# Performance work log

Hardware: AMD Instinct MI355X
Metric: run time of the kernel (lower is better)

The kernel has to match this reference:

```python
import jax, jax.numpy as jnp
import numpy as np

C = 32
KSHAPE = (C, C, 3, 3)  # (C_out, C_in, kH, kW)
BN_EPS = 1e-5


def _binary_act(x):
    # forward: sign(x); backward: identity clipped to |x|<1 (STE)
    xc = jnp.clip(x, -1.0, 1.0)
    return jax.lax.stop_gradient(jnp.sign(x) - xc) + xc


def _binarize_weight(w_flat, shape):
    w = w_flat.reshape(shape)
    scale = jax.lax.stop_gradient(jnp.mean(jnp.abs(w)))  # global scalar scale, detached
    wc = jnp.clip(w, -1.0, 1.0)
    # forward: scale*sign(w); backward flows through clamp(w,-1,1)
    return jax.lax.stop_gradient(scale * jnp.sign(w) - wc) + wc


def _bi_conv_bn(x, w_flat, gamma, beta, stride):
    xb = _binary_act(x)
    w = _binarize_weight(w_flat, KSHAPE)
    y = jax.lax.conv_general_dilated(
        xb, w, window_strides=(stride, stride), padding=[(1, 1), (1, 1)],
        dimension_numbers=('NCHW', 'OIHW', 'NCHW'))
    # BatchNorm2d in training mode (batch stats, biased variance)
    m = jnp.mean(y, axis=(0, 2, 3), keepdims=True)
    v = jnp.mean((y - m) ** 2, axis=(0, 2, 3), keepdims=True)
    yhat = (y - m) * jax.lax.rsqrt(v + BN_EPS)
    return gamma.reshape(1, -1, 1, 1) * yhat + beta.reshape(1, -1, 1, 1)


def setup_inputs() -> dict:
    key = jax.random.key(0)
    k1, k2, k3 = jax.random.split(key, 3)
    return {
        'x': jax.random.normal(k1, (32, C, 160, 160), dtype=jnp.float32),
        'w1': jax.random.normal(k2, (C * C * 9, 1), dtype=jnp.float32) * 0.05,
        'gamma1': jnp.ones((C,), dtype=jnp.float32),
        'beta1': jnp.zeros((C,), dtype=jnp.float32),
        'w2': jax.random.normal(k3, (C * C * 9, 1), dtype=jnp.float32) * 0.05,
        'gamma2': jnp.ones((C,), dtype=jnp.float32),
        'beta2': jnp.zeros((C,), dtype=jnp.float32),
    }


def reference(x, w1, gamma1, beta1, w2, gamma2, beta2):
    # bireal residual block, stride=1 => skip_op is Identity
    inner = _bi_conv_bn(x, w1, gamma1, beta1, 1) + x
    out = _bi_conv_bn(inner, w2, gamma2, beta2, 1) + inner
    return out
```

## Files before the change

kernel.cpp:

```cpp
#include <hip/hip_runtime.h>
#include <stdint.h>

#define NIMG 32
#define CH 32
#define HH 160
#define WW 160
#define HWL (HH*WW)
#define PRS 164
#define PHH 162
#define PIMG (PHH*PRS)
#define NPIX (NIMG*HWL)
#define HALO_WORDS 968

#define OFF_P     0
#define OFF_P2    3400704
#define OFF_INNER (OFF_P2 + 3400704)
#define OFF_WP    (OFF_INNER + 52428800)
#define OFF_CORR  (OFF_WP + 2304)
#define OFF_SC    (OFF_CORR + 2304)
#define OFF_SB    (OFF_SC + 128)

struct StatLine {
  int s1; int pad0; unsigned long long s2; char pad[112];
};

#define AS1 __attribute__((address_space(1)))
#define AS3 __attribute__((address_space(3)))
__device__ __forceinline__ void dma16(const void* g, void* l) {
  __builtin_amdgcn_global_load_lds((const AS1 void*)g, (AS3 void*)l, 16, 0, 0);
}

__device__ __forceinline__ unsigned short f2bf(float f) {
  unsigned u = __float_as_uint(f);
  u += 0x7fffu + ((u >> 16) & 1u);
  return (unsigned short)(u >> 16);
}
__device__ __forceinline__ float bf2f(unsigned short u) {
  return __uint_as_float((uint32_t)u << 16);
}

__device__ __forceinline__ void conv4(const uint32_t r[3][6], const uint32_t* wsh,
                                      int co, int& a0, int& a1, int& a2, int& a3)
{
  a0 = a1 = a2 = a3 = 0;
  #pragma unroll
  for (int dy = 0; dy < 3; ++dy) {
    #pragma unroll
    for (int dx = 0; dx < 3; ++dx) {
      uint32_t wvv = wsh[co * 9 + dy * 3 + dx];
      a0 += __popc(r[dy][0 + dx] ^ wvv);
      a1 += __popc(r[dy][1 + dx] ^ wvv);
      a2 += __popc(r[dy][2 + dx] ^ wvv);
      a3 += __popc(r[dy][3 + dx] ^ wvv);
    }
  }
}

__global__ __launch_bounds__(256) void pack_prep(const float* __restrict__ x,
    const float* __restrict__ w1, const float* __restrict__ w2,
    uint32_t* __restrict__ P, uint32_t* __restrict__ P2, uint32_t* __restrict__ WP,
    int* __restrict__ CORR, float* __restrict__ SC, StatLine* __restrict__ SB)
{
  __shared__ float lds[8192];
  const int tid = threadIdx.x;
  const int b = blockIdx.x;

  if (b >= 3200) {
    if (b == 3442) {
      int* z = (int*)SB;
      for (int i = tid; i < 2048; i += 256) z[i] = 0;
      float* red = lds;
      uint32_t* wpl = (uint32_t*)(lds + 256);
      for (int cv = 0; cv < 2; ++cv) {
        const float* w = cv ? w2 : w1;
        float s = 0.f;
        #pragma unroll
        for (int j = 0; j < 9; ++j) {
          float4 v = *reinterpret_cast<const float4*>(w + (j * 256 + tid) * 4);
          s += fabsf(v.x) + fabsf(v.y) + fabsf(v.z) + fabsf(v.w);
        }
        red[tid] = s;
        __syncthreads();
        for (int st = 128; st > 0; st >>= 1) {
          if (tid < st) red[tid] += red[tid + st];
          __syncthreads();
        }
        if (tid == 0) SC[cv] = red[0] / 9216.0f;
        for (int i = tid; i < 288; i += 256) {
          int co = i / 9, t = i - co * 9;
          uint32_t bw = 0;
          for (int ci = 0; ci < 32; ++ci)
            bw |= (w[(co * 32 + ci) * 9 + t] > 0.0f) ? (1u << ci) : 0u;
          WP[cv * 288 + i] = bw;
          wpl[i] = bw;
        }
        __syncthreads();
        for (int i = tid; i < 288; i += 256) {
          int cls = i / 32, co = i - cls * 32;
          int hc = cls / 3, wc = cls - hc * 3;
          int corr = 0;
          for (int t = 0; t < 9; ++t) {
            int dy = t / 3 - 1, dx = t % 3 - 1;
            bool inval = (hc == 0 && dy == -1) || (hc == 2 && dy == 1) ||
                         (wc == 0 && dx == -1) || (wc == 2 && dx == 1);
            if (inval) corr += 32 - 2 * __popc(wpl[co * 9 + t]);
          }
          CORR[cv * 288 + cls * 32 + co] = corr;
        }
        __syncthreads();
      }
    } else {
      int k = (b - 3200) * 256 + tid;
      uint32_t* buf = (k < 32 * HALO_WORDS) ? P : P2;
      int j = k % (32 * HALO_WORDS);
      int img = j / HALO_WORDS;
      int r = j - img * HALO_WORDS;
      int pr, pc;
      if (r < 164)      { pr = 0;   pc = r; }
      else if (r < 328) { pr = 161; pc = r - 164; }
      else {
        int k2 = r - 328;
        pr = 1 + (k2 >> 2);
        int q = k2 & 3;
        pc = (q == 0) ? 0 : (160 + q);
      }
      buf[img * PIMG + pr * PRS + pc] = 0;
    }
    return;
  }

  int n = b / 100;
  int p0 = (b - n * 100) * 256;
  const float* xb = x + (size_t)n * CH * HWL + p0;
  #pragma unroll
  for (int it = 0; it < 8; ++it) {
    int c = it * 4 + (tid >> 6);
    const float* g = xb + (size_t)c * HWL + (tid & 63) * 4;
    dma16(g, lds + c * 256);
  }
  __syncthreads();

  uint32_t bits = 0;
  #pragma unroll
  for (int c = 0; c < 32; ++c) {
    if (lds[c * 256 + tid] > 0.f) bits |= 1u << c;
  }
  int px = p0 + tid;
  int h = px / WW, w = px - h * WW;
  P[n * PIMG + (h + 1) * PRS + (w + 1)] = bits;
}

__global__ __launch_bounds__(256) void conv_stats(const uint32_t* __restrict__ P,
    const uint32_t* __restrict__ WP, const int* __restrict__ CORR,
    StatLine* __restrict__ sb)
{
  __shared__ uint32_t wsh[288];
  __shared__ int csh[288];
  __shared__ int ls1[32], ls2[32];
  const int tid = threadIdx.x;
  for (int i = tid; i < 288; i += 256) { wsh[i] = WP[i]; csh[i] = CORR[i]; }
  if (tid < 32) { ls1[tid] = 0; ls2[tid] = 0; }
  __syncthreads();

  int g = blockIdx.x * 256 + tid;
  int w4 = g % 40;
  int t1 = g / 40;
  int h = t1 % 160;
  int n = t1 / 160;

  const uint32_t* base = P + n * PIMG + h * PRS + w4 * 4;
  uint32_t r[3][6];
  #pragma unroll
  for (int dy = 0; dy < 3; ++dy) {
    uint4 a = *reinterpret_cast<const uint4*>(base + dy * PRS);
    uint2 bw = *reinterpret_cast<const uint2*>(base + dy * PRS + 4);
    r[dy][0] = a.x; r[dy][1] = a.y; r[dy][2] = a.z; r[dy][3] = a.w;
    r[dy][4] = bw.x; r[dy][5] = bw.y;
  }

  int rowc = (h == 0) ? 0 : ((h == 159) ? 6 : 3);
  int cls0  = rowc + ((w4 == 0) ? 0 : 1);
  int cls12 = rowc + 1;
  int cls3  = rowc + ((w4 == 39) ? 2 : 1);
  int lane = tid & 63;

  #pragma unroll
  for (int co = 0; co < 32; ++co) {
    int a0, a1, a2, a3;
    conv4(r, wsh, co, a0, a1, a2, a3);
    int d0 = 288 - 2 * a0 - csh[cls0 * 32 + co];
    int d1 = 288 - 2 * a1 - csh[cls12 * 32 + co];
    int d2 = 288 - 2 * a2 - csh[cls12 * 32 + co];
    int d3 = 288 - 2 * a3 - csh[cls3 * 32 + co];
    int ds = d0 + d1 + d2 + d3;
    int sq = d0 * d0 + d1 * d1 + d2 * d2 + d3 * d3;
    #pragma unroll
    for (int off = 32; off > 0; off >>= 1) {
      ds += __shfl_down(ds, off);
      sq += __shfl_down(sq, off);
    }
    if (lane == 0) { atomicAdd(&ls1[co], ds); atomicAdd(&ls2[co], sq); }
  }
  __syncthreads();
  if (tid < 32) {
    atomicAdd(&sb[tid].s1, ls1[tid]);
    atomicAdd(&sb[tid].s2, (unsigned long long)(long long)ls2[tid]);
  }
}

__global__ __launch_bounds__(256, 2) void conv_bn1(const uint32_t* __restrict__ P,
    const uint32_t* __restrict__ WP, const int* __restrict__ CORR,
    const float* __restrict__ x, const float* __restrict__ SCp,
    const StatLine* __restrict__ sb, const float* __restrict__ gamma,
    const float* __restrict__ beta, unsigned short* __restrict__ INNER,
    uint32_t* __restrict__ P2)
{
  __shared__ uint32_t wsh[288];
  __shared__ int csh[288];
  __shared__ float Ash[32], Bsh[32];
  const int tid = threadIdx.x;
  for (int i = tid; i < 288; i += 256) { wsh[i] = WP[i]; csh[i] = CORR[i]; }
  if (tid < 32) {
    double sc = (double)SCp[0];
    double m  = sc * (double)sb[tid].s1 / (double)NPIX;
    double ms = sc * sc * (double)(long long)sb[tid].s2 / (double)NPIX;
    float inv = (float)(1.0 / sqrt(ms - m * m + 1e-5));
    float gm = gamma[tid];
    Ash[tid] = gm * inv * (float)sc;
    Bsh[tid] = beta[tid] - gm * inv * (float)m;
  }
  __syncthreads();

  int g = blockIdx.x * 256 + tid;
  int w4 = g % 40;
  int t1 = g / 40;
  int h = t1 % 160;
  int n = t1 / 160;

  const uint32_t* base = P + n * PIMG + h * PRS + w4 * 4;
  uint32_t r[3][6];
  #pragma unroll
  for (int dy = 0; dy < 3; ++dy) {
    uint4 a = *reinterpret_cast<const uint4*>(base + dy * PRS);
    uint2 bw = *reinterpret_cast<const uint2*>(base + dy * PRS + 4);
    r[dy][0] = a.x; r[dy][1] = a.y; r[dy][2] = a.z; r[dy][3] = a.w;
    r[dy][4] = bw.x; r[dy][5] = bw.y;
  }
  int rowc = (h == 0) ? 0 : ((h == 159) ? 6 : 3);
  int cls0  = rowc + ((w4 == 0) ? 0 : 1);
  int cls12 = rowc + 1;
  int cls3  = rowc + ((w4 == 39) ? 2 : 1);

  int i = h * WW + w4 * 4;
  size_t pbase = (size_t)n * CH * HWL + i;

  float4 xv[32];
  #pragma unroll
  for (int j = 0; j < 32; ++j)
    xv[j] = *reinterpret_cast<const float4*>(x + pbase + (size_t)j * HWL);

  uint32_t bb0 = 0, bb1 = 0, bb2 = 0, bb3 = 0;
  #pragma unroll
  for (int co = 0; co < 32; ++co) {
    int a0, a1, a2, a3;
    conv4(r, wsh, co, a0, a1, a2, a3);
    int d0 = 288 - 2 * a0 - csh[cls0 * 32 + co];
    int d1 = 288 - 2 * a1 - csh[cls12 * 32 + co];
    int d2 = 288 - 2 * a2 - csh[cls12 * 32 + co];
    int d3 = 288 - 2 * a3 - csh[cls3 * 32 + co];
    float A = Ash[co], Bv = Bsh[co];
    float v0 = fmaf(A, (float)d0, Bv) + xv[co].x;
    float v1 = fmaf(A, (float)d1, Bv) + xv[co].y;
    float v2 = fmaf(A, (float)d2, Bv) + xv[co].z;
    float v3 = fmaf(A, (float)d3, Bv) + xv[co].w;
    ushort4 o; o.x = f2bf(v0); o.y = f2bf(v1); o.z = f2bf(v2); o.w = f2bf(v3);
    *reinterpret_cast<ushort4*>(INNER + pbase + (size_t)co * HWL) = o;
    uint32_t m = 1u << co;
    if (v0 > 0.f) bb0 |= m;
    if (v1 > 0.f) bb1 |= m;
    if (v2 > 0.f) bb2 |= m;
    if (v3 > 0.f) bb3 |= m;
  }
  uint32_t* pw = P2 + n * PIMG + (h + 1) * PRS + (w4 * 4 + 1);
  pw[0] = bb0; pw[1] = bb1; pw[2] = bb2; pw[3] = bb3;
}

__global__ __launch_bounds__(256, 2) void conv_bn2(const uint32_t* __restrict__ P2,
    const uint32_t* __restrict__ WP, const int* __restrict__ CORR,
    const unsigned short* __restrict__ INNER, const float* __restrict__ SCp,
    const StatLine* __restrict__ sb, const float* __restrict__ gamma,
    const float* __restrict__ beta, float* __restrict__ out)
{
  __shared__ uint32_t wsh[288];
  __shared__ int csh[288];
  __shared__ float Ash[32], Bsh[32];
  const int tid = threadIdx.x;
  for (int i = tid; i < 288; i += 256) { wsh[i] = WP[i]; csh[i] = CORR[i]; }
  if (tid < 32) {
    double sc = (double)SCp[0];
    double m  = sc * (double)sb[tid].s1 / (double)NPIX;
    double ms = sc * sc * (double)(long long)sb[tid].s2 / (double)NPIX;
    float inv = (float)(1.0 / sqrt(ms - m * m + 1e-5));
    float gm = gamma[tid];
    Ash[tid] = gm * inv * (float)sc;
    Bsh[tid] = beta[tid] - gm * inv * (float)m;
  }
  __syncthreads();

  int g = blockIdx.x * 256 + tid;
  int w4 = g % 40;
  int t1 = g / 40;
  int h = t1 % 160;
  int n = t1 / 160;

  const uint32_t* base = P2 + n * PIMG + h * PRS + w4 * 4;
  uint32_t r[3][6];
  #pragma unroll
  for (int dy = 0; dy < 3; ++dy) {
    uint4 a = *reinterpret_cast<const uint4*>(base + dy * PRS);
    uint2 bw = *reinterpret_cast<const uint2*>(base + dy * PRS + 4);
    r[dy][0] = a.x; r[dy][1] = a.y; r[dy][2] = a.z; r[dy][3] = a.w;
    r[dy][4] = bw.x; r[dy][5] = bw.y;
  }
  int rowc = (h == 0) ? 0 : ((h == 159) ? 6 : 3);
  int cls0  = rowc + ((w4 == 0) ? 0 : 1);
  int cls12 = rowc + 1;
  int cls3  = rowc + ((w4 == 39) ? 2 : 1);

  int i = h * WW + w4 * 4;
  size_t pbase = (size_t)n * CH * HWL + i;

  ushort4 iv[32];
  #pragma unroll
  for (int j = 0; j < 32; ++j)
    iv[j] = *reinterpret_cast<const ushort4*>(INNER + pbase + (size_t)j * HWL);

  #pragma unroll
  for (int co = 0; co < 32; ++co) {
    int a0, a1, a2, a3;
    conv4(r, wsh, co, a0, a1, a2, a3);
    int d0 = 288 - 2 * a0 - csh[cls0 * 32 + co];
    int d1 = 288 - 2 * a1 - csh[cls12 * 32 + co];
    int d2 = 288 - 2 * a2 - csh[cls12 * 32 + co];
    int d3 = 288 - 2 * a3 - csh[cls3 * 32 + co];
    float A = Ash[co], Bv = Bsh[co];
    float4 o;
    o.x = fmaf(A, (float)d0, Bv) + bf2f(iv[co].x);
    o.y = fmaf(A, (float)d1, Bv) + bf2f(iv[co].y);
    o.z = fmaf(A, (float)d2, Bv) + bf2f(iv[co].z);
    o.w = fmaf(A, (float)d3, Bv) + bf2f(iv[co].w);
    *reinterpret_cast<float4*>(out + pbase + (size_t)co * HWL) = o;
  }
}

extern "C" void kernel_launch(void* const* d_in, const int* in_sizes, int n_in,
                              void* d_out, int out_size, void* d_ws, size_t ws_size,
                              hipStream_t stream)
{
  (void)in_sizes; (void)n_in; (void)out_size; (void)ws_size;
  const float* x  = (const float*)d_in[0];
  const float* w1 = (const float*)d_in[1];
  const float* g1 = (const float*)d_in[2];
  const float* b1 = (const float*)d_in[3];
  const float* w2 = (const float*)d_in[4];
  const float* g2 = (const float*)d_in[5];
  const float* b2 = (const float*)d_in[6];
  float* out = (float*)d_out;
  char* ws = (char*)d_ws;

  uint32_t*       P     = (uint32_t*)(ws + OFF_P);
  uint32_t*       P2    = (uint32_t*)(ws + OFF_P2);
  unsigned short* INNER = (unsigned short*)(ws + OFF_INNER);
  uint32_t*       WP    = (uint32_t*)(ws + OFF_WP);
  int*            CORR  = (int*)(ws + OFF_CORR);
  float*          SC    = (float*)(ws + OFF_SC);
  StatLine*       SB    = (StatLine*)(ws + OFF_SB);

  pack_prep<<<3443, 256, 0, stream>>>(x, w1, w2, P, P2, WP, CORR, SC, SB);
  conv_stats<<<800, 256, 0, stream>>>(P, WP, CORR, SB);
  conv_bn1<<<800, 256, 0, stream>>>(P, WP, CORR, x, SC, SB, g1, b1, INNER, P2);
  conv_stats<<<800, 256, 0, stream>>>(P2, WP + 288, CORR + 288, SB + 32);
  conv_bn2<<<800, 256, 0, stream>>>(P2, WP + 288, CORR + 288, INNER, SC + 1, SB + 32, g2, b2, out);
}
```

Baseline: 176.1 us.

## Fuse all stages into one persistent kernel with grid barriers, keep inner in registers

Replaces the five separate launches with a single persistent kernel of 800 blocks. Four software grid barriers built on atomic counters separate the stages. Each thread owns the same pixels across all stages, so the bf16 inner activation stays in registers instead of being written to and read back from a 52MB global buffer, and the x reload for the residual is spread over channel groups. The cost is spin-wait barriers that deadlock unless all 800 blocks are resident at once, which launch bounds of 4 blocks per CU are meant to ensure. Register pressure also rises from holding 32 ushort4 values across the barriers.

```diff
diff --git a/kernel.cpp b/kernel.cpp
--- a/kernel.cpp
+++ b/kernel.cpp
@@ -11,14 +11,15 @@
 #define PIMG (PHH*PRS)
 #define NPIX (NIMG*HWL)
 #define HALO_WORDS 968
+#define NBLK 800
 
 #define OFF_P     0
 #define OFF_P2    3400704
-#define OFF_INNER (OFF_P2 + 3400704)
-#define OFF_WP    (OFF_INNER + 52428800)
+#define OFF_WP    (OFF_P2 + 3400704)
 #define OFF_CORR  (OFF_WP + 2304)
 #define OFF_SC    (OFF_CORR + 2304)
 #define OFF_SB    (OFF_SC + 128)
+#define OFF_CNT   (OFF_SB + 8192)
 
 struct StatLine {
   int s1; int pad0; unsigned long long s2; char pad[112];
@@ -56,133 +57,153 @@
   }
 }
 
-__global__ __launch_bounds__(256) void pack_prep(const float* __restrict__ x,
-    const float* __restrict__ w1, const float* __restrict__ w2,
-    uint32_t* __restrict__ P, uint32_t* __restrict__ P2, uint32_t* __restrict__ WP,
-    int* __restrict__ CORR, float* __restrict__ SC, StatLine* __restrict__ SB)
+__device__ __forceinline__ void gridbar(int* cnt) {
+  __syncthreads();
+  if (threadIdx.x == 0) {
+    __threadfence();
+    atomicAdd(cnt, 1);
+    int it = 0;
+    while (__hip_atomic_load(cnt, __ATOMIC_ACQUIRE, __HIP_MEMORY_SCOPE_AGENT) < NBLK) {
+      __builtin_amdgcn_s_sleep(16);
+      if (++it > (1 << 28)) break;
+    }
+    __threadfence();
+  }
+  __syncthreads();
+}
+
+__global__ __launch_bounds__(256, 4) void mega(
+    const float* __restrict__ x,
+    const float* __restrict__ w1, const float* __restrict__ g1, const float* __restrict__ b1,
+    const float* __restrict__ w2, const float* __restrict__ g2, const float* __restrict__ b2,
+    uint32_t* __restrict__ P, uint32_t* __restrict__ P2,
+    uint32_t* __restrict__ WP, int* __restrict__ CORR, float* __restrict__ SC,
+    StatLine* __restrict__ SB, int* __restrict__ cnt, float* __restrict__ out)
 {
   __shared__ float lds[8192];
+  __shared__ uint32_t wsh[288];
+  __shared__ int csh[288];
+  __shared__ float Ash[32], Bsh[32];
   const int tid = threadIdx.x;
   const int b = blockIdx.x;
 
-  if (b >= 3200) {
-    if (b == 3442) {
-      int* z = (int*)SB;
-      for (int i = tid; i < 2048; i += 256) z[i] = 0;
-      float* red = lds;
-      uint32_t* wpl = (uint32_t*)(lds + 256);
-      for (int cv = 0; cv < 2; ++cv) {
-        const float* w = cv ? w2 : w1;
-        float s = 0.f;
-        #pragma unroll
-        for (int j = 0; j < 9; ++j) {
-          float4 v = *reinterpret_cast<const float4*>(w + (j * 256 + tid) * 4);
-          s += fabsf(v.x) + fabsf(v.y) + fabsf(v.z) + fabsf(v.w);
+  if (b < 242) {
+    int k = b * 256 + tid;
+    uint32_t* buf = (k < 32 * HALO_WORDS) ? P : P2;
+    int j = k % (32 * HALO_WORDS);
+    int img = j / HALO_WORDS;
+    int r = j - img * HALO_WORDS;
+    int pr, pc;
+    if (r < 164)      { pr = 0;   pc = r; }
+    else if (r < 328) { pr = 161; pc = r - 164; }
+    else {
+      int k2 = r - 328;
+      pr = 1 + (k2 >> 2);
+      int q = k2 & 3;
+      pc = (q == 0) ? 0 : (160 + q);
+    }
+    buf[img * PIMG + pr * PRS + pc] = 0;
+  }
+
+  {
+    int n = b / 25;
+    int base_px = (b - n * 25) * 1024;
+    for (int s = 0; s < 4; ++s) {
+      int p0 = base_px + s * 256;
+      const float* xb = x + (size_t)n * CH * HWL + p0;
+      #pragma unroll
+      for (int it = 0; it < 8; ++it) {
+        int c = it * 4 + (tid >> 6);
+        dma16(xb + (size_t)c * HWL + (tid & 63) * 4, lds + c * 256);
+      }
+      __syncthreads();
+      uint32_t bits = 0;
+      #pragma unroll
+      for (int c = 0; c < 32; ++c)
+        if (lds[c * 256 + tid] > 0.f) bits |= 1u << c;
+      int px = p0 + tid;
+      int h = px / WW, w = px - (px / WW) * WW;
+      P[n * PIMG + (h + 1) * PRS + (w + 1)] = bits;
+      __syncthreads();
+    }
+  }
+
+  if (b == NBLK - 1) {
+    int* z = (int*)SB;
+    for (int i = tid; i < 2048; i += 256) z[i] = 0;
+    float* red = lds;
+    uint32_t* wpl = (uint32_t*)(lds + 256);
+    for (int cv = 0; cv < 2; ++cv) {
+      const float* w = cv ? w2 : w1;
+      float s = 0.f;
+      #pragma unroll
+      for (int j = 0; j < 9; ++j) {
+        float4 v = *reinterpret_cast<const float4*>(w + (j * 256 + tid) * 4);
+        s += fabsf(v.x) + fabsf(v.y) + fabsf(v.z) + fabsf(v.w);
+      }
+      red[tid] = s;
+      __syncthreads();
+      for (int st = 128; st > 0; st >>= 1) {
+        if (tid < st) red[tid] += red[tid + st];
+        __syncthreads();
+      }
+      if (tid == 0) SC[cv] = red[0] / 9216.0f;
+      for (int i = tid; i < 288; i += 256) {
+        int co = i / 9, t = i - co * 9;
+        uint32_t bw = 0;
+        for (int ci = 0; ci < 32; ++ci)
+          bw |= (w[(co * 32 + ci) * 9 + t] > 0.0f) ? (1u << ci) : 0u;
+        WP[cv * 288 + i] = bw;
+        wpl[i] = bw;
+      }
+      __syncthreads();
+      for (int i = tid; i < 288; i += 256) {
+        int cls = i / 32, co = i - cls * 32;
+        int hc = cls / 3, wc = cls - hc * 3;
+        int corr = 0;
+        for (int t = 0; t < 9; ++t) {
+          int dy = t / 3 - 1, dx = t % 3 - 1;
+          bool inval = (hc == 0 && dy == -1) || (hc == 2 && dy == 1) ||
+                       (wc == 0 && dx == -1) || (wc == 2 && dx == 1);
+          if (inval) corr += 32 - 2 * __popc(wpl[co * 9 + t]);
         }
-        red[tid] = s;
-        __syncthreads();
-        for (int st = 128; st > 0; st >>= 1) {
-          if (tid < st) red[tid] += red[tid + st];
-          __syncthreads();
-        }
-        if (tid == 0) SC[cv] = red[0] / 9216.0f;
-        for (int i = tid; i < 288; i += 256) {
-          int co = i / 9, t = i - co * 9;
-          uint32_t bw = 0;
-          for (int ci = 0; ci < 32; ++ci)
-            bw |= (w[(co * 32 + ci) * 9 + t] > 0.0f) ? (1u << ci) : 0u;
-          WP[cv * 288 + i] = bw;
-          wpl[i] = bw;
-        }
-        __syncthreads();
-        for (int i = tid; i < 288; i += 256) {
-          int cls = i / 32, co = i - cls * 32;
-          int hc = cls / 3, wc = cls - hc * 3;
-          int corr = 0;
-          for (int t = 0; t < 9; ++t) {
-            int dy = t / 3 - 1, dx = t % 3 - 1;
-            bool inval = (hc == 0 && dy == -1) || (hc == 2 && dy == 1) ||
-                         (wc == 0 && dx == -1) || (wc == 2 && dx == 1);
-            if (inval) corr += 32 - 2 * __popc(wpl[co * 9 + t]);
-          }
-          CORR[cv * 288 + cls * 32 + co] = corr;
-        }
-        __syncthreads();
-      }
-    } else {
-      int k = (b - 3200) * 256 + tid;
-      uint32_t* buf = (k < 32 * HALO_WORDS) ? P : P2;
-      int j = k % (32 * HALO_WORDS);
-      int img = j / HALO_WORDS;
-      int r = j - img * HALO_WORDS;
-      int pr, pc;
-      if (r < 164)      { pr = 0;   pc = r; }
-      else if (r < 328) { pr = 161; pc = r - 164; }
-      else {
-        int k2 = r - 328;
-        pr = 1 + (k2 >> 2);
-        int q = k2 & 3;
-        pc = (q == 0) ? 0 : (160 + q);
-      }
-      buf[img * PIMG + pr * PRS + pc] = 0;
-    }
-    return;
-  }
-
-  int n = b / 100;
-  int p0 = (b - n * 100) * 256;
-  const float* xb = x + (size_t)n * CH * HWL + p0;
-  #pragma unroll
-  for (int it = 0; it < 8; ++it) {
-    int c = it * 4 + (tid >> 6);
-    const float* g = xb + (size_t)c * HWL + (tid & 63) * 4;
-    dma16(g, lds + c * 256);
-  }
-  __syncthreads();
-
-  uint32_t bits = 0;
-  #pragma unroll
-  for (int c = 0; c < 32; ++c) {
-    if (lds[c * 256 + tid] > 0.f) bits |= 1u << c;
-  }
-  int px = p0 + tid;
-  int h = px / WW, w = px - h * WW;
-  P[n * PIMG + (h + 1) * PRS + (w + 1)] = bits;
-}
-
-__global__ __launch_bounds__(256) void conv_stats(const uint32_t* __restrict__ P,
-    const uint32_t* __restrict__ WP, const int* __restrict__ CORR,
-    StatLine* __restrict__ sb)
-{
-  __shared__ uint32_t wsh[288];
-  __shared__ int csh[288];
-  __shared__ int ls1[32], ls2[32];
-  const int tid = threadIdx.x;
-  for (int i = tid; i < 288; i += 256) { wsh[i] = WP[i]; csh[i] = CORR[i]; }
-  if (tid < 32) { ls1[tid] = 0; ls2[tid] = 0; }
-  __syncthreads();
-
-  int g = blockIdx.x * 256 + tid;
+        CORR[cv * 288 + cls * 32 + co] = corr;
+      }
+      __syncthreads();
+    }
+  }
+
+  gridbar(cnt + 0);
+
+  int g = b * 256 + tid;
   int w4 = g % 40;
   int t1 = g / 40;
   int h = t1 % 160;
-  int n = t1 / 160;
-
-  const uint32_t* base = P + n * PIMG + h * PRS + w4 * 4;
-  uint32_t r[3][6];
-  #pragma unroll
-  for (int dy = 0; dy < 3; ++dy) {
-    uint4 a = *reinterpret_cast<const uint4*>(base + dy * PRS);
-    uint2 bw = *reinterpret_cast<const uint2*>(base + dy * PRS + 4);
-    r[dy][0] = a.x; r[dy][1] = a.y; r[dy][2] = a.z; r[dy][3] = a.w;
-    r[dy][4] = bw.x; r[dy][5] = bw.y;
-  }
-
+  int n2 = t1 / 160;
   int rowc = (h == 0) ? 0 : ((h == 159) ? 6 : 3);
   int cls0  = rowc + ((w4 == 0) ? 0 : 1);
   int cls12 = rowc + 1;
   int cls3  = rowc + ((w4 == 39) ? 2 : 1);
+  size_t pbase = (size_t)n2 * CH * HWL + h * WW + w4 * 4;
   int lane = tid & 63;
+
+  int* ls1 = (int*)lds;
+  int* ls2 = (int*)lds + 32;
+  for (int i = tid; i < 288; i += 256) { wsh[i] = WP[i]; csh[i] = CORR[i]; }
+  if (tid < 32) { ls1[tid] = 0; ls2[tid] = 0; }
+  __syncthreads();
+
+  uint32_t r[3][6];
+  {
+    const uint32_t* bp = P + n2 * PIMG + h * PRS + w4 * 4;
+    #pragma unroll
+    for (int dy = 0; dy < 3; ++dy) {
+      uint4 a = *reinterpret_cast<const uint4*>(bp + dy * PRS);
+      uint2 bw = *reinterpret_cast<const uint2*>(bp + dy * PRS + 4);
+      r[dy][0] = a.x; r[dy][1] = a.y; r[dy][2] = a.z; r[dy][3] = a.w;
+      r[dy][4] = bw.x; r[dy][5] = bw.y;
+    }
+  }
 
   #pragma unroll
   for (int co = 0; co < 32; ++co) {
@@ -203,63 +224,74 @@
   }
   __syncthreads();
   if (tid < 32) {
-    atomicAdd(&sb[tid].s1, ls1[tid]);
-    atomicAdd(&sb[tid].s2, (unsigned long long)(long long)ls2[tid]);
-  }
-}
-
-__global__ __launch_bounds__(256, 2) void conv_bn1(const uint32_t* __restrict__ P,
-    const uint32_t* __restrict__ WP, const int* __restrict__ CORR,
-    const float* __restrict__ x, const float* __restrict__ SCp,
-    const StatLine* __restrict__ sb, const float* __restrict__ gamma,
-    const float* __restrict__ beta, unsigned short* __restrict__ INNER,
-    uint32_t* __restrict__ P2)
-{
-  __shared__ uint32_t wsh[288];
-  __shared__ int csh[288];
-  __shared__ float Ash[32], Bsh[32];
-  const int tid = threadIdx.x;
-  for (int i = tid; i < 288; i += 256) { wsh[i] = WP[i]; csh[i] = CORR[i]; }
+    atomicAdd(&SB[tid].s1, ls1[tid]);
+    atomicAdd(&SB[tid].s2, (unsigned long long)(long long)ls2[tid]);
+  }
+
+  gridbar(cnt + 1);
+
   if (tid < 32) {
-    double sc = (double)SCp[0];
-    double m  = sc * (double)sb[tid].s1 / (double)NPIX;
-    double ms = sc * sc * (double)(long long)sb[tid].s2 / (double)NPIX;
+    double sc = (double)SC[0];
+    double m  = sc * (double)SB[tid].s1 / (double)NPIX;
+    double ms = sc * sc * (double)(long long)SB[tid].s2 / (double)NPIX;
     float inv = (float)(1.0 / sqrt(ms - m * m + 1e-5));
-    float gm = gamma[tid];
+    float gm = g1[tid];
     Ash[tid] = gm * inv * (float)sc;
-    Bsh[tid] = beta[tid] - gm * inv * (float)m;
-  }
-  __syncthreads();
-
-  int g = blockIdx.x * 256 + tid;
-  int w4 = g % 40;
-  int t1 = g / 40;
-  int h = t1 % 160;
-  int n = t1 / 160;
-
-  const uint32_t* base = P + n * PIMG + h * PRS + w4 * 4;
-  uint32_t r[3][6];
-  #pragma unroll
-  for (int dy = 0; dy < 3; ++dy) {
-    uint4 a = *reinterpret_cast<const uint4*>(base + dy * PRS);
-    uint2 bw = *reinterpret_cast<const uint2*>(base + dy * PRS + 4);
-    r[dy][0] = a.x; r[dy][1] = a.y; r[dy][2] = a.z; r[dy][3] = a.w;
-    r[dy][4] = bw.x; r[dy][5] = bw.y;
-  }
-  int rowc = (h == 0) ? 0 : ((h == 159) ? 6 : 3);
-  int cls0  = rowc + ((w4 == 0) ? 0 : 1);
-  int cls12 = rowc + 1;
-  int cls3  = rowc + ((w4 == 39) ? 2 : 1);
-
-  int i = h * WW + w4 * 4;
-  size_t pbase = (size_t)n * CH * HWL + i;
-
-  float4 xv[32];
-  #pragma unroll
-  for (int j = 0; j < 32; ++j)
-    xv[j] = *reinterpret_cast<const float4*>(x + pbase + (size_t)j * HWL);
-
+    Bsh[tid] = b1[tid] - gm * inv * (float)m;
+  }
+  __syncthreads();
+
+  ushort4 iv[32];
   uint32_t bb0 = 0, bb1 = 0, bb2 = 0, bb3 = 0;
+  #pragma unroll
+  for (int cg = 0; cg < 4; ++cg) {
+    float4 xv[8];
+    #pragma unroll
+    for (int j = 0; j < 8; ++j)
+      xv[j] = *reinterpret_cast<const float4*>(x + pbase + (size_t)(cg * 8 + j) * HWL);
+    #pragma unroll
+    for (int j = 0; j < 8; ++j) {
+      int co = cg * 8 + j;
+      int a0, a1, a2, a3;
+      conv4(r, wsh, co, a0, a1, a2, a3);
+      int d0 = 288 - 2 * a0 - csh[cls0 * 32 + co];
+      int d1 = 288 - 2 * a1 - csh[cls12 * 32 + co];
+      int d2 = 288 - 2 * a2 - csh[cls12 * 32 + co];
+      int d3 = 288 - 2 * a3 - csh[cls3 * 32 + co];
+      float A = Ash[co], Bv = Bsh[co];
+      float v0 = fmaf(A, (float)d0, Bv) + xv[j].x;
+      float v1 = fmaf(A, (float)d1, Bv) + xv[j].y;
+      float v2 = fmaf(A, (float)d2, Bv) + xv[j].z;
+      float v3 = fmaf(A, (float)d3, Bv) + xv[j].w;
+      ushort4 o; o.x = f2bf(v0); o.y = f2bf(v1); o.z = f2bf(v2); o.w = f2bf(v3);
+      iv[co] = o;
+      uint32_t m = 1u << co;
+      if (v0 > 0.f) bb0 |= m;
+      if (v1 > 0.f) bb1 |= m;
+      if (v2 > 0.f) bb2 |= m;
+      if (v3 > 0.f) bb3 |= m;
+    }
+  }
+  {
+    uint32_t* pw = P2 + n2 * PIMG + (h + 1) * PRS + (w4 * 4 + 1);
+    pw[0] = bb0; pw[1] = bb1; pw[2] = bb2; pw[3] = bb3;
+  }
+
+  gridbar(cnt + 2);
+
+  for (int i = tid; i < 288; i += 256) { wsh[i] = WP[288 + i]; csh[i] = CORR[288 + i]; }
+  if (tid < 32) { ls1[tid] = 0; ls2[tid] = 0; }
+  __syncthreads();
+  {
+    const uint32_t* bp = P2 + n2 * PIMG + h * PRS + w4 * 4;
+    #pragma unroll
+    for (int dy = 0; dy < 3; ++dy) {
+      uint4 a = *reinterpret_cast<const uint4*>(bp + dy * PRS);
+      uint2 bw = *reinterpret_cast<const uint2*>(bp + dy * PRS + 4);
+      r[dy][0] = a.x; r[dy][1] = a.y; r[dy][2] = a.z; r[dy][3] = a.w;
+      r[dy][4] = bw.x; r[dy][5] = bw.y;
+    }
+  }
   #pragma unroll
   for (int co = 0; co < 32; ++co) {
     int a0, a1, a2, a3;
@@ -268,72 +300,33 @@
     int d1 = 288 - 2 * a1 - csh[cls12 * 32 + co];
     int d2 = 288 - 2 * a2 - csh[cls12 * 32 + co];
     int d3 = 288 - 2 * a3 - csh[cls3 * 32 + co];
-    float A = Ash[co], Bv = Bsh[co];
-    float v0 = fmaf(A, (float)d0, Bv) + xv[co].x;
-    float v1 = fmaf(A, (float)d1, Bv) + xv[co].y;
-    float v2 = fmaf(A, (float)d2, Bv) + xv[co].z;
-    float v3 = fmaf(A, (float)d3, Bv) + xv[co].w;
-    ushort4 o; o.x = f2bf(v0); o.y = f2bf(v1); o.z = f2bf(v2); o.w = f2bf(v3);
-    *reinterpret_cast<ushort4*>(INNER + pbase + (size_t)co * HWL) = o;
-    uint32_t m = 1u << co;
-    if (v0 > 0.f) bb0 |= m;
-    if (v1 > 0.f) bb1 |= m;
-    if (v2 > 0.f) bb2 |= m;
-    if (v3 > 0.f) bb3 |= m;
-  }
-  uint32_t* pw = P2 + n * PIMG + (h + 1) * PRS + (w4 * 4 + 1);
-  pw[0] = bb0; pw[1] = bb1; pw[2] = bb2; pw[3] = bb3;
-}
-
-__global__ __launch_bounds__(256, 2) void conv_bn2(const uint32_t* __restrict__ P2,
-    const uint32_t* __restrict__ WP, const int* __restrict__ CORR,
-    const unsigned short* __restrict__ INNER, const float* __restrict__ SCp,
-    const StatLine* __restrict__ sb, const float* __restrict__ gamma,
-    const float* __restrict__ beta, float* __restrict__ out)
-{
-  __shared__ uint32_t wsh[288];
-  __shared__ int csh[288];
-  __shared__ float Ash[32], Bsh[32];
-  const int tid = threadIdx.x;
-  for (int i = tid; i < 288; i += 256) { wsh[i] = WP[i]; csh[i] = CORR[i]; }
+    int ds = d0 + d1 + d2 + d3;
+    int sq = d0 * d0 + d1 * d1 + d2 * d2 + d3 * d3;
+    #pragma unroll
+    for (int off = 32; off > 0; off >>= 1) {
+      ds += __shfl_down(ds, off);
+      sq += __shfl_down(sq, off);
+    }
+    if (lane == 0) { atomicAdd(&ls1[co], ds); atomicAdd(&ls2[co], sq); }
+  }
+  __syncthreads();
   if (tid < 32) {
-    double sc = (double)SCp[0];
-    double m  = sc * (double)sb[tid].s1 / (double)NPIX;
-    double ms = sc * sc * (double)(long long)sb[tid].s2 / (double)NPIX;
+    atomicAdd(&SB[32 + tid].s1, ls1[tid]);
+    atomicAdd(&SB[32 + tid].s2, (unsigned long long)(long long)ls2[tid]);
+  }
+
+  gridbar(cnt + 3);
+
+  if (tid < 32) {
+    double sc = (double)SC[1];
+    double m  = sc * (double)SB[32 + tid].s1 / (double)NPIX;
+    double ms = sc * sc * (double)(long long)SB[32 + tid].s2 / (double)NPIX;
     float inv = (float)(1.0 / sqrt(ms - m * m + 1e-5));
-    float gm = gamma[tid];
+    float gm = g2[tid];
     Ash[tid] = gm * inv * (float)sc;
-    Bsh[tid] = beta[tid] - gm * inv * (float)m;
-  }
-  __syncthreads();
-
-  int g = blockIdx.x * 256 + tid;
-  int w4 = g % 40;
-  int t1 = g / 40;
-  int h = t1 % 160;
-  int n = t1 / 160;
-
-  const uint32_t* base = P2 + n * PIMG + h * PRS + w4 * 4;
-  uint32_t r[3][6];
-  #pragma unroll
-  for (int dy = 0; dy < 3; ++dy) {
-    uint4 a = *reinterpret_cast<const uint4*>(base + dy * PRS);
-    uint2 bw = *reinterpret_cast<const uint2*>(base + dy * PRS + 4);
-    r[dy][0] = a.x; r[dy][1] = a.y; r[dy][2] = a.z; r[dy][3] = a.w;
-    r[dy][4] = bw.x; r[dy][5] = bw.y;
-  }
-  int rowc = (h == 0) ? 0 : ((h == 159) ? 6 : 3);
-  int cls0  = rowc + ((w4 == 0) ? 0 : 1);
-  int cls12 = rowc + 1;
-  int cls3  = rowc + ((w4 == 39) ? 2 : 1);
-
-  int i = h * WW + w4 * 4;
-  size_t pbase = (size_t)n * CH * HWL + i;
-
-  ushort4 iv[32];
-  #pragma unroll
-  for (int j = 0; j < 32; ++j)
-    iv[j] = *reinterpret_cast<const ushort4*>(INNER + pbase + (size_t)j * HWL);
+    Bsh[tid] = b2[tid] - gm * inv * (float)m;
+  }
+  __syncthreads();
 
   #pragma unroll
   for (int co = 0; co < 32; ++co) {
@@ -368,17 +361,15 @@
   float* out = (float*)d_out;
   char* ws = (char*)d_ws;
 
-  uint32_t*       P     = (uint32_t*)(ws + OFF_P);
-  uint32_t*       P2    = (uint32_t*)(ws + OFF_P2);
-  unsigned short* INNER = (unsigned short*)(ws + OFF_INNER);
-  uint32_t*       WP    = (uint32_t*)(ws + OFF_WP);
-  int*            CORR  = (int*)(ws + OFF_CORR);
-  float*          SC    = (float*)(ws + OFF_SC);
-  StatLine*       SB    = (StatLine*)(ws + OFF_SB);
-
-  pack_prep<<<3443, 256, 0, stream>>>(x, w1, w2, P, P2, WP, CORR, SC, SB);
-  conv_stats<<<800, 256, 0, stream>>>(P, WP, CORR, SB);
-  conv_bn1<<<800, 256, 0, stream>>>(P, WP, CORR, x, SC, SB, g1, b1, INNER, P2);
-  conv_stats<<<800, 256, 0, stream>>>(P2, WP + 288, CORR + 288, SB + 32);
-  conv_bn2<<<800, 256, 0, stream>>>(P2, WP + 288, CORR + 288, INNER, SC + 1, SB + 32, g2, b2, out);
-}
+  uint32_t* P    = (uint32_t*)(ws + OFF_P);
+  uint32_t* P2   = (uint32_t*)(ws + OFF_P2);
+  uint32_t* WP   = (uint32_t*)(ws + OFF_WP);
+  int*      CORR = (int*)(ws + OFF_CORR);
+  float*    SC   = (float*)(ws + OFF_SC);
+  StatLine* SB   = (StatLine*)(ws + OFF_SB);
+  int*      CNT  = (int*)(ws + OFF_CNT);
+
+  hipMemsetAsync(CNT, 0, 4 * sizeof(int), stream);
+  mega<<<NBLK, 256, 0, stream>>>(x, w1, g1, b1, w2, g2, b2,
+                                 P, P2, WP, CORR, SC, SB, CNT, out);
+}
```

Measured after the change: 677.3 us. 3.85x slower.

## Recompute first conv in final kernel instead of storing bf16 inner tensor

Applied to the files above, without the earlier changes.

Removes the bf16 INNER intermediate. conv_bn1 now only emits the sign bits P2. The final kernel recomputes the first binary conv+BN from P and re-reads x to rebuild the residual, then adds the second conv+BN. This trades roughly 100 MB of bf16 write and read traffic for an extra popcount conv and a second 200 MB fp32 read of x. It also loads x in 8-channel chunks to limit register pressure. As a side effect, the residual is now full fp32 rather than bf16-rounded.

```diff
diff --git a/kernel.cpp b/kernel.cpp
--- a/kernel.cpp
+++ b/kernel.cpp
@@ -14,8 +14,7 @@
 
 #define OFF_P     0
 #define OFF_P2    3400704
-#define OFF_INNER (OFF_P2 + 3400704)
-#define OFF_WP    (OFF_INNER + 52428800)
+#define OFF_WP    (OFF_P2 + 3400704)
 #define OFF_CORR  (OFF_WP + 2304)
 #define OFF_SC    (OFF_CORR + 2304)
 #define OFF_SB    (OFF_SC + 128)
@@ -28,15 +27,6 @@
 #define AS3 __attribute__((address_space(3)))
 __device__ __forceinline__ void dma16(const void* g, void* l) {
   __builtin_amdgcn_global_load_lds((const AS1 void*)g, (AS3 void*)l, 16, 0, 0);
-}
-
-__device__ __forceinline__ unsigned short f2bf(float f) {
-  unsigned u = __float_as_uint(f);
-  u += 0x7fffu + ((u >> 16) & 1u);
-  return (unsigned short)(u >> 16);
-}
-__device__ __forceinline__ float bf2f(unsigned short u) {
-  return __uint_as_float((uint32_t)u << 16);
 }
 
 __device__ __forceinline__ void conv4(const uint32_t r[3][6], const uint32_t* wsh,
@@ -135,8 +125,7 @@
   #pragma unroll
   for (int it = 0; it < 8; ++it) {
     int c = it * 4 + (tid >> 6);
-    const float* g = xb + (size_t)c * HWL + (tid & 63) * 4;
-    dma16(g, lds + c * 256);
+    dma16(xb + (size_t)c * HWL + (tid & 63) * 4, lds + c * 256);
   }
   __syncthreads();
 
@@ -212,8 +201,7 @@
     const uint32_t* __restrict__ WP, const int* __restrict__ CORR,
     const float* __restrict__ x, const float* __restrict__ SCp,
     const StatLine* __restrict__ sb, const float* __restrict__ gamma,
-    const float* __restrict__ beta, unsigned short* __restrict__ INNER,
-    uint32_t* __restrict__ P2)
+    const float* __restrict__ beta, uint32_t* __restrict__ P2)
 {
   __shared__ uint32_t wsh[288];
   __shared__ int csh[288];
@@ -254,56 +242,66 @@
   int i = h * WW + w4 * 4;
   size_t pbase = (size_t)n * CH * HWL + i;
 
-  float4 xv[32];
-  #pragma unroll
-  for (int j = 0; j < 32; ++j)
-    xv[j] = *reinterpret_cast<const float4*>(x + pbase + (size_t)j * HWL);
-
   uint32_t bb0 = 0, bb1 = 0, bb2 = 0, bb3 = 0;
   #pragma unroll
-  for (int co = 0; co < 32; ++co) {
-    int a0, a1, a2, a3;
-    conv4(r, wsh, co, a0, a1, a2, a3);
-    int d0 = 288 - 2 * a0 - csh[cls0 * 32 + co];
-    int d1 = 288 - 2 * a1 - csh[cls12 * 32 + co];
-    int d2 = 288 - 2 * a2 - csh[cls12 * 32 + co];
-    int d3 = 288 - 2 * a3 - csh[cls3 * 32 + co];
-    float A = Ash[co], Bv = Bsh[co];
-    float v0 = fmaf(A, (float)d0, Bv) + xv[co].x;
-    float v1 = fmaf(A, (float)d1, Bv) + xv[co].y;
-    float v2 = fmaf(A, (float)d2, Bv) + xv[co].z;
-    float v3 = fmaf(A, (float)d3, Bv) + xv[co].w;
-    ushort4 o; o.x = f2bf(v0); o.y = f2bf(v1); o.z = f2bf(v2); o.w = f2bf(v3);
-    *reinterpret_cast<ushort4*>(INNER + pbase + (size_t)co * HWL) = o;
-    uint32_t m = 1u << co;
-    if (v0 > 0.f) bb0 |= m;
-    if (v1 > 0.f) bb1 |= m;
-    if (v2 > 0.f) bb2 |= m;
-    if (v3 > 0.f) bb3 |= m;
+  for (int cg = 0; cg < 4; ++cg) {
+    float4 xv[8];
+    #pragma unroll
+    for (int j = 0; j < 8; ++j)
+      xv[j] = *reinterpret_cast<const float4*>(x + pbase + (size_t)(cg * 8 + j) * HWL);
+    #pragma unroll
+    for (int j = 0; j < 8; ++j) {
+      int co = cg * 8 + j;
+      int a0, a1, a2, a3;
+      conv4(r, wsh, co, a0, a1, a2, a3);
+      int d0 = 288 - 2 * a0 - csh[cls0 * 32 + co];
+      int d1 = 288 - 2 * a1 - csh[cls12 * 32 + co];
+      int d2 = 288 - 2 * a2 - csh[cls12 * 32 + co];
+      int d3 = 288 - 2 * a3 - csh[cls3 * 32 + co];
+      float A = Ash[co], Bv = Bsh[co];
+      float v0 = fmaf(A, (float)d0, Bv) + xv[j].x;
+      float v1 = fmaf(A, (float)d1, Bv) + xv[j].y;
+      float v2 = fmaf(A, (float)d2, Bv) + xv[j].z;
+      float v3 = fmaf(A, (float)d3, Bv) + xv[j].w;
+      uint32_t m = 1u << co;
+      if (v0 > 0.f) bb0 |= m;
+      if (v1 > 0.f) bb1 |= m;
+      if (v2 > 0.f) bb2 |= m;
+      if (v3 > 0.f) bb3 |= m;
+    }
   }
   uint32_t* pw = P2 + n * PIMG + (h + 1) * PRS + (w4 * 4 + 1);
   pw[0] = bb0; pw[1] = bb1; pw[2] = bb2; pw[3] = bb3;
 }
 
-__global__ __launch_bounds__(256, 2) void conv_bn2(const uint32_t* __restrict__ P2,
-    const uint32_t* __restrict__ WP, const int* __restrict__ CORR,
-    const unsigned short* __restrict__ INNER, const float* __restrict__ SCp,
-    const StatLine* __restrict__ sb, const float* __restrict__ gamma,
-    const float* __restrict__ beta, float* __restrict__ out)
-{
-  __shared__ uint32_t wsh[288];
-  __shared__ int csh[288];
-  __shared__ float Ash[32], Bsh[32];
+__global__ __launch_bounds__(256, 2) void conv_bn2(const uint32_t* __restrict__ P,
+    const uint32_t* __restrict__ P2, const uint32_t* __restrict__ WP,
+    const int* __restrict__ CORR, const float* __restrict__ x,
+    const float* __restrict__ SC, const StatLine* __restrict__ SB,
+    const float* __restrict__ g1v, const float* __restrict__ b1v,
+    const float* __restrict__ g2v, const float* __restrict__ b2v,
+    float* __restrict__ out)
+{
+  __shared__ uint32_t wsh[576];
+  __shared__ int csh[576];
+  __shared__ float A1s[32], B1s[32], A2s[32], B2s[32];
   const int tid = threadIdx.x;
-  for (int i = tid; i < 288; i += 256) { wsh[i] = WP[i]; csh[i] = CORR[i]; }
+  for (int i = tid; i < 576; i += 256) { wsh[i] = WP[i]; csh[i] = CORR[i]; }
   if (tid < 32) {
-    double sc = (double)SCp[0];
-    double m  = sc * (double)sb[tid].s1 / (double)NPIX;
-    double ms = sc * sc * (double)(long long)sb[tid].s2 / (double)NPIX;
+    double sc = (double)SC[0];
+    double m  = sc * (double)SB[tid].s1 / (double)NPIX;
+    double ms = sc * sc * (double)(long long)SB[tid].s2 / (double)NPIX;
     float inv = (float)(1.0 / sqrt(ms - m * m + 1e-5));
-    float gm = gamma[tid];
-    Ash[tid] = gm * inv * (float)sc;
-    Bsh[tid] = beta[tid] - gm * inv * (float)m;
+    float gm = g1v[tid];
+    A1s[tid] = gm * inv * (float)sc;
+    B1s[tid] = b1v[tid] - gm * inv * (float)m;
+    double sc2 = (double)SC[1];
+    double m2  = sc2 * (double)SB[32 + tid].s1 / (double)NPIX;
+    double ms2 = sc2 * sc2 * (double)(long long)SB[32 + tid].s2 / (double)NPIX;
+    float inv2 = (float)(1.0 / sqrt(ms2 - m2 * m2 + 1e-5));
+    float gm2 = g2v[tid];
+    A2s[tid] = gm2 * inv2 * (float)sc2;
+    B2s[tid] = b2v[tid] - gm2 * inv2 * (float)m2;
   }
   __syncthreads();
 
@@ -313,14 +311,21 @@
   int h = t1 % 160;
   int n = t1 / 160;
 
-  const uint32_t* base = P2 + n * PIMG + h * PRS + w4 * 4;
-  uint32_t r[3][6];
-  #pragma unroll
-  for (int dy = 0; dy < 3; ++dy) {
-    uint4 a = *reinterpret_cast<const uint4*>(base + dy * PRS);
-    uint2 bw = *reinterpret_cast<const uint2*>(base + dy * PRS + 4);
-    r[dy][0] = a.x; r[dy][1] = a.y; r[dy][2] = a.z; r[dy][3] = a.w;
-    r[dy][4] = bw.x; r[dy][5] = bw.y;
+  uint32_t r1[3][6], r2[3][6];
+  {
+    const uint32_t* b1p = P  + n * PIMG + h * PRS + w4 * 4;
+    const uint32_t* b2p = P2 + n * PIMG + h * PRS + w4 * 4;
+    #pragma unroll
+    for (int dy = 0; dy < 3; ++dy) {
+      uint4 a = *reinterpret_cast<const uint4*>(b1p + dy * PRS);
+      uint2 bw = *reinterpret_cast<const uint2*>(b1p + dy * PRS + 4);
+      r1[dy][0] = a.x; r1[dy][1] = a.y; r1[dy][2] = a.z; r1[dy][3] = a.w;
+      r1[dy][4] = bw.x; r1[dy][5] = bw.y;
+      uint4 c = *reinterpret_cast<const uint4*>(b2p + dy * PRS);
+      uint2 dw = *reinterpret_cast<const uint2*>(b2p + dy * PRS + 4);
+      r2[dy][0] = c.x; r2[dy][1] = c.y; r2[dy][2] = c.z; r2[dy][3] = c.w;
+      r2[dy][4] = dw.x; r2[dy][5] = dw.y;
+    }
   }
   int rowc = (h == 0) ? 0 : ((h == 159) ? 6 : 3);
   int cls0  = rowc + ((w4 == 0) ? 0 : 1);
@@ -330,26 +335,38 @@
   int i = h * WW + w4 * 4;
   size_t pbase = (size_t)n * CH * HWL + i;
 
-  ushort4 iv[32];
-  #pragma unroll
-  for (int j = 0; j < 32; ++j)
-    iv[j] = *reinterpret_cast<const ushort4*>(INNER + pbase + (size_t)j * HWL);
-
-  #pragma unroll
-  for (int co = 0; co < 32; ++co) {
-    int a0, a1, a2, a3;
-    conv4(r, wsh, co, a0, a1, a2, a3);
-    int d0 = 288 - 2 * a0 - csh[cls0 * 32 + co];
-    int d1 = 288 - 2 * a1 - csh[cls12 * 32 + co];
-    int d2 = 288 - 2 * a2 - csh[cls12 * 32 + co];
-    int d3 = 288 - 2 * a3 - csh[cls3 * 32 + co];
-    float A = Ash[co], Bv = Bsh[co];
-    float4 o;
-    o.x = fmaf(A, (float)d0, Bv) + bf2f(iv[co].x);
-    o.y = fmaf(A, (float)d1, Bv) + bf2f(iv[co].y);
-    o.z = fmaf(A, (float)d2, Bv) + bf2f(iv[co].z);
-    o.w = fmaf(A, (float)d3, Bv) + bf2f(iv[co].w);
-    *reinterpret_cast<float4*>(out + pbase + (size_t)co * HWL) = o;
+  #pragma unroll
+  for (int cg = 0; cg < 4; ++cg) {
+    float4 xv[8];
+    #pragma unroll
+    for (int j = 0; j < 8; ++j)
+      xv[j] = *reinterpret_cast<const float4*>(x + pbase + (size_t)(cg * 8 + j) * HWL);
+    #pragma unroll
+    for (int j = 0; j < 8; ++j) {
+      int co = cg * 8 + j;
+      int a0, a1, a2, a3, e0, e1, e2, e3;
+      conv4(r1, wsh, co, a0, a1, a2, a3);
+      conv4(r2, wsh + 288, co, e0, e1, e2, e3);
+      int d0 = 288 - 2 * a0 - csh[cls0 * 32 + co];
+      int d1 = 288 - 2 * a1 - csh[cls12 * 32 + co];
+      int d2 = 288 - 2 * a2 - csh[cls12 * 32 + co];
+      int d3 = 288 - 2 * a3 - csh[cls3 * 32 + co];
+      int f0 = 288 - 2 * e0 - csh[288 + cls0 * 32 + co];
+      int f1 = 288 - 2 * e1 - csh[288 + cls12 * 32 + co];
+      int f2 = 288 - 2 * e2 - csh[288 + cls12 * 32 + co];
+      int f3 = 288 - 2 * e3 - csh[288 + cls3 * 32 + co];
+      float A1 = A1s[co], B1 = B1s[co], A2 = A2s[co], B2 = B2s[co];
+      float v0 = fmaf(A1, (float)d0, B1) + xv[j].x;
+      float v1 = fmaf(A1, (float)d1, B1) + xv[j].y;
+      float v2 = fmaf(A1, (float)d2, B1) + xv[j].z;
+      float v3 = fmaf(A1, (float)d3, B1) + xv[j].w;
+      float4 o;
+      o.x = fmaf(A2, (float)f0, B2) + v0;
+      o.y = fmaf(A2, (float)f1, B2) + v1;
+      o.z = fmaf(A2, (float)f2, B2) + v2;
+      o.w = fmaf(A2, (float)f3, B2) + v3;
+      *reinterpret_cast<float4*>(out + pbase + (size_t)co * HWL) = o;
+    }
   }
 }
 
@@ -368,17 +385,16 @@
   float* out = (float*)d_out;
   char* ws = (char*)d_ws;
 
-  uint32_t*       P     = (uint32_t*)(ws + OFF_P);
-  uint32_t*       P2    = (uint32_t*)(ws + OFF_P2);
-  unsigned short* INNER = (unsigned short*)(ws + OFF_INNER);
-  uint32_t*       WP    = (uint32_t*)(ws + OFF_WP);
-  int*            CORR  = (int*)(ws + OFF_CORR);
-  float*          SC    = (float*)(ws + OFF_SC);
-  StatLine*       SB    = (StatLine*)(ws + OFF_SB);
+  uint32_t* P    = (uint32_t*)(ws + OFF_P);
+  uint32_t* P2   = (uint32_t*)(ws + OFF_P2);
+  uint32_t* WP   = (uint32_t*)(ws + OFF_WP);
+  int*      CORR = (int*)(ws + OFF_CORR);
+  float*    SC   = (float*)(ws + OFF_SC);
+  StatLine* SB   = (StatLine*)(ws + OFF_SB);
 
   pack_prep<<<3443, 256, 0, stream>>>(x, w1, w2, P, P2, WP, CORR, SC, SB);
   conv_stats<<<800, 256, 0, stream>>>(P, WP, CORR, SB);
-  conv_bn1<<<800, 256, 0, stream>>>(P, WP, CORR, x, SC, SB, g1, b1, INNER, P2);
+  conv_bn1<<<800, 256, 0, stream>>>(P, WP, CORR, x, SC, SB, g1, b1, P2);
   conv_stats<<<800, 256, 0, stream>>>(P2, WP + 288, CORR + 288, SB + 32);
-  conv_bn2<<<800, 256, 0, stream>>>(P2, WP + 288, CORR + 288, INNER, SC + 1, SB + 32, g2, b2, out);
-}
+  conv_bn2<<<800, 256, 0, stream>>>(P, P2, WP, CORR, x, SC, SB, g1, b1, g2, b2, out);
+}
```

After: 194.7 us. +10.6%, slower.
